# Kernel tuning notes

Measured on AMD Instinct MI355X. Metric: run time of the kernel, lower is better.

The kernel has to match this reference:

```python
import jax, jax.numpy as jnp
import numpy as np

NLAYER = 4
H = 0.1


def tv_norm(X, eps=1e-3):
    # mean-center and L2-normalize each channel over the node/edge dim
    X = X - jnp.mean(X, axis=1, keepdims=True)
    return X / jnp.sqrt(jnp.sum(X * X, axis=1, keepdims=True) + eps)


def setup_inputs() -> dict:
    key = jax.random.key(0)
    ks = jax.random.split(key, 12)
    nIn, nopenN, nopenE, nclose = 128, 128, 128, 128
    nN, nE = 50000, 500000
    xn = jax.random.normal(ks[0], (nIn, nN), dtype=jnp.float32)
    xe = jax.random.normal(ks[1], (nIn, nE), dtype=jnp.float32)
    iInd = jax.random.randint(ks[2], (nE,), 0, nN)
    jInd = jax.random.randint(ks[3], (nE,), 0, nN)
    KNopen = jax.random.uniform(ks[4], (nopenN, nIn), dtype=jnp.float32) * 0.1
    KEopen = jax.random.uniform(ks[5], (nopenE, nIn), dtype=jnp.float32) * 0.1
    KNclose = jax.random.uniform(ks[6], (nclose, nopenN), dtype=jnp.float32) * 0.1
    KEclose = jax.random.uniform(ks[7], (nclose, nopenE), dtype=jnp.float32) * 0.1
    KN = jax.random.uniform(ks[8], (NLAYER, nopenE, nopenN), dtype=jnp.float32) * 0.001
    KE = jax.random.uniform(ks[9], (NLAYER, nopenN, nopenE), dtype=jnp.float32) * 0.001
    return {"xn": xn, "xe": xe, "iInd": iInd, "jInd": jInd,
            "KNopen": KNopen, "KEopen": KEopen, "KNclose": KNclose,
            "KEclose": KEclose, "KN": KN, "KE": KE}


def reference(xn, xe, iInd, jInd, KNopen, KEopen, KNclose, KEclose, KN, KE):
    nN = xn.shape[1]

    def node_grad(x):           # [d, nN] -> [d, nE]
        return x[:, iInd] - x[:, jInd]

    def edge_div(e):            # [d, nE] -> [d, nN]
        z = jnp.zeros((e.shape[0], nN), dtype=e.dtype)
        return z.at[:, iInd].add(e).at[:, jInd].add(-e)

    xn = KNopen @ xn            # [nopenN, nN]
    xe = KEopen @ xe            # [nopenE, nE]
    for i in range(NLAYER):
        Ai = tv_norm(KN[i] @ node_grad(xn))          # [nopenE, nE]
        xe = xe + H * jax.nn.relu(Ai)
        Bi = tv_norm(jax.nn.relu(KE[i] @ edge_div(xe)))  # [nopenN, nN]
        xn = xn + H * jax.nn.relu(Bi)
    xn = KNclose @ xn
    xe = KNclose @ xe  # note: original code uses KNclose for xe as well
    return (xn, xe)
```

## Files before the change

kernel.cpp:

```cpp
#include <hip/hip_runtime.h>


#define HSTEP 0.1f
#define TVEPS 1e-3f

typedef __attribute__((ext_vector_type(8))) short short8v;
typedef __attribute__((ext_vector_type(4))) float f32x4;

__device__ inline float4 f4z() { return make_float4(0.f, 0.f, 0.f, 0.f); }

__device__ inline unsigned short f2bf(float x) {
  unsigned u = __float_as_uint(x);
  unsigned r = (u + 0x7fffu + ((u >> 16) & 1u)) >> 16;
  return (unsigned short)r;
}
__device__ inline float bf2f(unsigned short h) {
  return __uint_as_float(((unsigned)h) << 16);
}

__global__ __launch_bounds__(256) void pack6(const float* __restrict__ KNopen,
                                             const float* __restrict__ KEopen,
                                             const float* __restrict__ KN,
                                             unsigned short* __restrict__ dst) {
  const int idx = blockIdx.x * 256 + threadIdx.x;
  const int m = blockIdx.y;
  const int o = idx >> 7, k = idx & 127;
  const float* src;
  if (m == 0) src = KNopen;
  else if (m == 1) src = KEopen;
  else src = KN + (m - 2) * 16384;
  const float val = src[o * 128 + k];
  const unsigned short hi = f2bf(val);
  const unsigned short lo = f2bf(val - bf2f(hi));
  const int lane = (o & 15) + 16 * ((k >> 3) & 3);
  const int base =
      m * 32768 + (k >> 5) * 8192 + (o >> 4) * 512 + lane * 8 + (k & 7);
  dst[base] = hi;
  dst[base + 4096] = lo;
}

__global__ __launch_bounds__(256) void prep_close_w(
    const float* __restrict__ KNclose, const float* __restrict__ KEopen,
    unsigned short* __restrict__ Apack) {
  const int idx = blockIdx.x * 256 + threadIdx.x;
  const int p = idx >> 14, ok = idx & 16383;
  const int o = ok >> 7, k = ok & 127;
  float val;
  if (p == 0) {
    float s = 0.f;
    for (int m = 0; m < 128; ++m)
      s = fmaf(KNclose[o * 128 + m], KEopen[m * 128 + k], s);
    val = s;
  } else {
    val = KNclose[o * 128 + k];
  }
  const unsigned short hi = f2bf(val);
  const unsigned short lo = f2bf(val - bf2f(hi));
  const int chunk = p * 4 + (k >> 5);
  const int lane = (o & 15) + 16 * ((k >> 3) & 3);
  const int base = chunk * 8192 + (o >> 4) * 512 + lane * 8 + (k & 7);
  Apack[base] = hi;
  Apack[base + 4096] = lo;
}

__global__ __launch_bounds__(256, 2) void gemm_e_mfma(
    const float* __restrict__ X, const unsigned short* __restrict__ Wp,
    const int N, float* __restrict__ Yt) {
  __shared__ float4 Asf[1024];
  const int tid = threadIdx.x;
  const int l = tid & 63, w = tid >> 6;
  const int er = l & 15, kg = l >> 4;
  const long e0 = (long)blockIdx.x * 128;

  f32x4 acc[8][2];
#pragma unroll
  for (int of = 0; of < 8; ++of)
#pragma unroll
    for (int f = 0; f < 2; ++f) acc[of][f] = (f32x4){0.f, 0.f, 0.f, 0.f};

  long e_f[2];
  bool ev[2];
#pragma unroll
  for (int f = 0; f < 2; ++f) {
    long e = e0 + 32 * w + 16 * f + er;
    ev[f] = (e < N);
    e_f[f] = ev[f] ? e : (long)(N - 1);
  }

  const short8v* Ap = (const short8v*)Asf;

  for (int ks = 0; ks < 4; ++ks) {
    const float4* src = (const float4*)Wp + ks * 1024;
    __syncthreads();
    Asf[tid] = src[tid];
    Asf[tid + 256] = src[tid + 256];
    Asf[tid + 512] = src[tid + 512];
    Asf[tid + 768] = src[tid + 768];
    __syncthreads();

    short8v bh[2], bl[2];
#pragma unroll
    for (int f = 0; f < 2; ++f) {
      const float* col = X + e_f[f];
      const int kbase = 32 * ks + 8 * kg;
      float xv[8];
#pragma unroll
      for (int j = 0; j < 8; ++j) xv[j] = col[(long)(kbase + j) * N];
#pragma unroll
      for (int j = 0; j < 8; ++j) {
        const unsigned short h = f2bf(xv[j]);
        const unsigned short lo = f2bf(xv[j] - bf2f(h));
        bh[f][j] = (short)h;
        bl[f][j] = (short)lo;
      }
    }

#pragma unroll
    for (int of = 0; of < 8; ++of) {
      const short8v ah = Ap[of * 64 + l];
      const short8v al = Ap[512 + of * 64 + l];
#pragma unroll
      for (int f = 0; f < 2; ++f) {
        acc[of][f] =
            __builtin_amdgcn_mfma_f32_16x16x32_bf16(ah, bh[f], acc[of][f], 0, 0, 0);
        acc[of][f] =
            __builtin_amdgcn_mfma_f32_16x16x32_bf16(ah, bl[f], acc[of][f], 0, 0, 0);
        acc[of][f] =
            __builtin_amdgcn_mfma_f32_16x16x32_bf16(al, bh[f], acc[of][f], 0, 0, 0);
      }
    }
  }

#pragma unroll
  for (int of = 0; of < 8; ++of) {
#pragma unroll
    for (int f = 0; f < 2; ++f) {
      if (!ev[f]) continue;
      *(f32x4*)&Yt[e_f[f] * 128 + of * 16 + 4 * kg] = acc[of][f];
    }
  }
}

template <int MODE>
__global__ __launch_bounds__(256, 2) void gemm_n_mfma(
    const float* __restrict__ X, const unsigned short* __restrict__ Wp,
    const int N, float* __restrict__ Y) {
  __shared__ float4 Asf[1024];
  const int tid = threadIdx.x;
  const int l = tid & 63, w = tid >> 6;
  const int er = l & 15, kg = l >> 4;
  const long n0 = (long)blockIdx.x * 128;

  f32x4 acc[8][2];
#pragma unroll
  for (int of = 0; of < 8; ++of)
#pragma unroll
    for (int f = 0; f < 2; ++f) acc[of][f] = (f32x4){0.f, 0.f, 0.f, 0.f};

  long n_f[2];
  bool nv[2];
#pragma unroll
  for (int f = 0; f < 2; ++f) {
    long n = n0 + 32 * w + 16 * f + er;
    nv[f] = (n < N);
    n_f[f] = nv[f] ? n : (long)(N - 1);
  }

  const short8v* Ap = (const short8v*)Asf;

  for (int ks = 0; ks < 4; ++ks) {
    const float4* src = (const float4*)Wp + ks * 1024;
    __syncthreads();
    Asf[tid] = src[tid];
    Asf[tid + 256] = src[tid + 256];
    Asf[tid + 512] = src[tid + 512];
    Asf[tid + 768] = src[tid + 768];
    __syncthreads();

    short8v bh[2], bl[2];
#pragma unroll
    for (int f = 0; f < 2; ++f) {
      const float* row = X + n_f[f] * 128 + 32 * ks + 8 * kg;
      const float4 v0 = *(const float4*)row;
      const float4 v1 = *(const float4*)(row + 4);
      float xv[8] = {v0.x, v0.y, v0.z, v0.w, v1.x, v1.y, v1.z, v1.w};
#pragma unroll
      for (int j = 0; j < 8; ++j) {
        const unsigned short h = f2bf(xv[j]);
        const unsigned short lo = f2bf(xv[j] - bf2f(h));
        bh[f][j] = (short)h;
        bl[f][j] = (short)lo;
      }
    }

#pragma unroll
    for (int of = 0; of < 8; ++of) {
      const short8v ah = Ap[of * 64 + l];
      const short8v al = Ap[512 + of * 64 + l];
#pragma unroll
      for (int f = 0; f < 2; ++f) {
        acc[of][f] =
            __builtin_amdgcn_mfma_f32_16x16x32_bf16(ah, bh[f], acc[of][f], 0, 0, 0);
        acc[of][f] =
            __builtin_amdgcn_mfma_f32_16x16x32_bf16(ah, bl[f], acc[of][f], 0, 0, 0);
        acc[of][f] =
            __builtin_amdgcn_mfma_f32_16x16x32_bf16(al, bh[f], acc[of][f], 0, 0, 0);
      }
    }
  }

  if (MODE == 0) {
#pragma unroll
    for (int of = 0; of < 8; ++of) {
#pragma unroll
      for (int f = 0; f < 2; ++f) {
        if (!nv[f]) continue;
        *(f32x4*)&Y[n_f[f] * 128 + of * 16 + 4 * kg] = acc[of][f];
      }
    }
  } else {
#pragma unroll
    for (int of = 0; of < 8; ++of) {
#pragma unroll
      for (int f = 0; f < 2; ++f) {
        if (!nv[f]) continue;
#pragma unroll
        for (int r = 0; r < 4; ++r) {
          const long o = of * 16 + 4 * kg + r;
          Y[o * N + n_f[f]] = acc[of][f][r];
        }
      }
    }
  }
}

__global__ __launch_bounds__(256, 2) void gemm_n1(
    const float* __restrict__ X, const float* __restrict__ Kmat, const int N,
    float* __restrict__ Y, float* __restrict__ statS,
    float* __restrict__ statQ) {
  __shared__ float Xs[64 * 33];
  __shared__ float Ks[32 * 132];
  __shared__ float red[2 * 128 * 17];
  const int tid = threadIdx.x;
  const int ng = tid & 15, og = tid >> 4;
  const long n0 = (long)blockIdx.x * 64;

  float acc[4][8];
#pragma unroll
  for (int q = 0; q < 4; ++q)
#pragma unroll
    for (int j = 0; j < 8; ++j) acc[q][j] = 0.f;

  for (int kc = 0; kc < 128; kc += 32) {
#pragma unroll
    for (int i = 0; i < 2; ++i) {
      int f4i = tid + 256 * i;
      int n = f4i >> 3, c4 = (f4i & 7) << 2;
      long gn = n0 + n;
      float4 v = f4z();
      if (gn < N) v = *(const float4*)&X[gn * 128 + kc + c4];
      Xs[n * 33 + c4 + 0] = v.x;
      Xs[n * 33 + c4 + 1] = v.y;
      Xs[n * 33 + c4 + 2] = v.z;
      Xs[n * 33 + c4 + 3] = v.w;
    }
#pragma unroll
    for (int i = 0; i < 4; ++i) {
      int f4i = tid + 256 * i;
      int o = f4i >> 3, c4 = (f4i & 7) << 2;
      float4 v = *(const float4*)&Kmat[o * 128 + kc + c4];
      Ks[(c4 + 0) * 132 + o] = v.x;
      Ks[(c4 + 1) * 132 + o] = v.y;
      Ks[(c4 + 2) * 132 + o] = v.z;
      Ks[(c4 + 3) * 132 + o] = v.w;
    }
    __syncthreads();
#pragma unroll
    for (int kk = 0; kk < 32; ++kk) {
      float xv[4];
#pragma unroll
      for (int q = 0; q < 4; ++q) xv[q] = Xs[(4 * ng + q) * 33 + kk];
      const float4 k0 = *(const float4*)&Ks[kk * 132 + 8 * og];
      const float4 k1 = *(const float4*)&Ks[kk * 132 + 8 * og + 4];
      float kv[8] = {k0.x, k0.y, k0.z, k0.w, k1.x, k1.y, k1.z, k1.w};
#pragma unroll
      for (int q = 0; q < 4; ++q)
#pragma unroll
        for (int j = 0; j < 8; ++j) acc[q][j] = fmaf(xv[q], kv[j], acc[q][j]);
    }
    __syncthreads();
  }

#pragma unroll
  for (int q = 0; q < 4; ++q)
#pragma unroll
    for (int j = 0; j < 8; ++j) acc[q][j] = fmaxf(acc[q][j], 0.f);
#pragma unroll
  for (int q = 0; q < 4; ++q) {
    long n = n0 + 4 * ng + q;
    if (n < N) {
      *(float4*)&Y[n * 128 + 8 * og] =
          make_float4(acc[q][0], acc[q][1], acc[q][2], acc[q][3]);
      *(float4*)&Y[n * 128 + 8 * og + 4] =
          make_float4(acc[q][4], acc[q][5], acc[q][6], acc[q][7]);
    }
  }
  float* redS = red;
  float* redQ = red + 128 * 17;
#pragma unroll
  for (int j = 0; j < 8; ++j) {
    int o = 8 * og + j;
    float s = acc[0][j] + acc[1][j] + acc[2][j] + acc[3][j];
    float qq = acc[0][j] * acc[0][j] + acc[1][j] * acc[1][j] +
               acc[2][j] * acc[2][j] + acc[3][j] * acc[3][j];
    redS[o * 17 + ng] = s;
    redQ[o * 17 + ng] = qq;
  }
  __syncthreads();
  if (tid < 128) {
    float s = 0.f, qq = 0.f;
#pragma unroll
    for (int g = 0; g < 16; ++g) {
      s += redS[tid * 17 + g];
      qq += redQ[tid * 17 + g];
    }
    atomicAdd(&statS[tid], s);
    atomicAdd(&statQ[tid], qq);
  }
}

__global__ __launch_bounds__(256, 2) void close_edge_mfma(
    const float* __restrict__ xe, const float* __restrict__ Sacc,
    const unsigned short* __restrict__ Apack, const int nE,
    float* __restrict__ out) {
  __shared__ float4 Asf[1024];
  const int tid = threadIdx.x;
  const int l = tid & 63, w = tid >> 6;
  const int er = l & 15;
  const int kg = l >> 4;
  const long e0 = (long)blockIdx.x * 128;

  f32x4 acc[8][2];
#pragma unroll
  for (int of = 0; of < 8; ++of)
#pragma unroll
    for (int f = 0; f < 2; ++f) acc[of][f] = (f32x4){0.f, 0.f, 0.f, 0.f};

  long e_f[2];
  bool ev[2];
#pragma unroll
  for (int f = 0; f < 2; ++f) {
    long e = e0 + 32 * w + 16 * f + er;
    ev[f] = (e < nE);
    e_f[f] = ev[f] ? e : (long)(nE - 1);
  }

  const short8v* Ap = (const short8v*)Asf;

  for (int p = 0; p < 2; ++p) {
    for (int ks = 0; ks < 4; ++ks) {
      const float4* src = (const float4*)Apack + (p * 4 + ks) * 1024;
      __syncthreads();
      Asf[tid] = src[tid];
      Asf[tid + 256] = src[tid + 256];
      Asf[tid + 512] = src[tid + 512];
      Asf[tid + 768] = src[tid + 768];
      __syncthreads();

      short8v bh[2], bl[2];
#pragma unroll
      for (int f = 0; f < 2; ++f) {
        float xv[8];
        if (p == 0) {
          const float* col = xe + e_f[f];
          const int kbase = 32 * ks + 8 * kg;
#pragma unroll
          for (int j = 0; j < 8; ++j) xv[j] = col[(long)(kbase + j) * nE];
        } else {
          const float* row = Sacc + e_f[f] * 128 + 32 * ks + 8 * kg;
          const float4 v0 = *(const float4*)row;
          const float4 v1 = *(const float4*)(row + 4);
          xv[0] = v0.x; xv[1] = v0.y; xv[2] = v0.z; xv[3] = v0.w;
          xv[4] = v1.x; xv[5] = v1.y; xv[6] = v1.z; xv[7] = v1.w;
        }
#pragma unroll
        for (int j = 0; j < 8; ++j) {
          const unsigned short h = f2bf(xv[j]);
          const unsigned short lo = f2bf(xv[j] - bf2f(h));
          bh[f][j] = (short)h;
          bl[f][j] = (short)lo;
        }
      }

#pragma unroll
      for (int of = 0; of < 8; ++of) {
        const short8v ah = Ap[of * 64 + l];
        const short8v al = Ap[512 + of * 64 + l];
#pragma unroll
        for (int f = 0; f < 2; ++f) {
          acc[of][f] =
              __builtin_amdgcn_mfma_f32_16x16x32_bf16(ah, bh[f], acc[of][f], 0, 0, 0);
          acc[of][f] =
              __builtin_amdgcn_mfma_f32_16x16x32_bf16(ah, bl[f], acc[of][f], 0, 0, 0);
          acc[of][f] =
              __builtin_amdgcn_mfma_f32_16x16x32_bf16(al, bh[f], acc[of][f], 0, 0, 0);
        }
      }
    }
  }

#pragma unroll
  for (int of = 0; of < 8; ++of) {
#pragma unroll
    for (int f = 0; f < 2; ++f) {
      if (!ev[f]) continue;
      const long e = e_f[f];
#pragma unroll
      for (int r = 0; r < 4; ++r) {
        const long o = of * 16 + 4 * kg + r;
        out[o * nE + e] = acc[of][f][r];
      }
    }
  }
}

__global__ __launch_bounds__(256) void count_deg(const int* __restrict__ iInd,
                                                 const int* __restrict__ jInd,
                                                 const int nE,
                                                 int* __restrict__ cnt) {
  const int e = blockIdx.x * 256 + threadIdx.x;
  if (e >= nE) return;
  atomicAdd(&cnt[iInd[e]], 1);
  atomicAdd(&cnt[jInd[e]], 1);
}

__global__ __launch_bounds__(1024) void scan_rowptr(const int* __restrict__ cnt,
                                                    int* __restrict__ rp,
                                                    const int nN) {
  __shared__ int buf[1024];
  __shared__ int carry;
  const int tid = threadIdx.x;
  if (tid == 0) {
    carry = 0;
    rp[0] = 0;
  }
  __syncthreads();
  for (int base = 0; base < nN; base += 1024) {
    int idx = base + tid;
    int v = (idx < nN) ? cnt[idx] : 0;
    buf[tid] = v;
    __syncthreads();
    for (int off = 1; off < 1024; off <<= 1) {
      int t = (tid >= off) ? buf[tid - off] : 0;
      __syncthreads();
      buf[tid] += t;
      __syncthreads();
    }
    if (idx < nN) rp[idx + 1] = buf[tid] + carry;
    __syncthreads();
    if (tid == 0) carry += buf[1023];
    __syncthreads();
  }
}

__global__ __launch_bounds__(256) void fill_adj(const int* __restrict__ iInd,
                                                const int* __restrict__ jInd,
                                                const int nE,
                                                const int* __restrict__ rp,
                                                int* __restrict__ cur,
                                                int* __restrict__ adj) {
  const int e = blockIdx.x * 256 + threadIdx.x;
  if (e >= nE) return;
  const int ii = iInd[e], jj = jInd[e];
  int s1 = atomicAdd(&cur[ii], 1);
  adj[rp[ii] + s1] = (e << 1);
  int s2 = atomicAdd(&cur[jj], 1);
  adj[rp[jj] + s2] = (e << 1) | 1;
}

template <bool OPEN>
__global__ __launch_bounds__(256) void div_gather(
    const float* __restrict__ E, const int* __restrict__ rp,
    const int* __restrict__ adj, const float* __restrict__ D0,
    float* __restrict__ D, const int nN) {
  const int cg = threadIdx.x & 31, slot = threadIdx.x >> 5;
  const long n = (long)blockIdx.x * 8 + slot;
  if (n >= nN) return;
  const float4* E4 = (const float4*)E;
  float4 acc;
  if (OPEN) {
    acc = f4z();
  } else {
    acc = ((const float4*)D0)[n * 32 + cg];
  }
  const int b = rp[n], en = rp[n + 1];
  for (int k = b; k < en; ++k) {
    const int ent = adj[k];
    const long e = ent >> 1;
    const float4 v = E4[e * 32 + cg];
    if (ent & 1) {
      acc.x -= v.x; acc.y -= v.y; acc.z -= v.z; acc.w -= v.w;
    } else {
      acc.x += v.x; acc.y += v.y; acc.z += v.z; acc.w += v.w;
    }
  }
  ((float4*)D)[n * 32 + cg] = acc;
}

__global__ __launch_bounds__(256) void edge_pass1(
    const float* __restrict__ W, const int* __restrict__ iInd,
    const int* __restrict__ jInd, const int nE, float* __restrict__ statS,
    float* __restrict__ statQ) {
  __shared__ float4 rs[256];
  __shared__ float4 rq[256];
  const int tid = threadIdx.x;
  const int cg = tid & 31, slot = tid >> 5;
  const float4* W4 = (const float4*)W;
  float4 s = f4z(), q = f4z();
  long start = (long)blockIdx.x * 512;
  long end = start + 512;
  if (end > nE) end = nE;
  for (long e = start + slot; e < end; e += 8) {
    const int ii = iInd[e], jj = jInd[e];
    const float4 wi = W4[(long)ii * 32 + cg];
    const float4 wj = W4[(long)jj * 32 + cg];
    const float y0 = wi.x - wj.x, y1 = wi.y - wj.y;
    const float y2 = wi.z - wj.z, y3 = wi.w - wj.w;
    s.x += y0; s.y += y1; s.z += y2; s.w += y3;
    q.x = fmaf(y0, y0, q.x); q.y = fmaf(y1, y1, q.y);
    q.z = fmaf(y2, y2, q.z); q.w = fmaf(y3, y3, q.w);
  }
  rs[tid] = s;
  rq[tid] = q;
  __syncthreads();
  if (tid < 32) {
    float4 S = rs[tid], Q = rq[tid];
#pragma unroll
    for (int g = 1; g < 8; ++g) {
      float4 a = rs[tid + 32 * g], b = rq[tid + 32 * g];
      S.x += a.x; S.y += a.y; S.z += a.z; S.w += a.w;
      Q.x += b.x; Q.y += b.y; Q.z += b.z; Q.w += b.w;
    }
    atomicAdd(&statS[tid * 4 + 0], S.x);
    atomicAdd(&statS[tid * 4 + 1], S.y);
    atomicAdd(&statS[tid * 4 + 2], S.z);
    atomicAdd(&statS[tid * 4 + 3], S.w);
    atomicAdd(&statQ[tid * 4 + 0], Q.x);
    atomicAdd(&statQ[tid * 4 + 1], Q.y);
    atomicAdd(&statQ[tid * 4 + 2], Q.z);
    atomicAdd(&statQ[tid * 4 + 3], Q.w);
  }
}

template <bool FIRST>
__global__ __launch_bounds__(256) void edge_pass2(
    const float* __restrict__ W, const int* __restrict__ iInd,
    const int* __restrict__ jInd, const int nE, const float* __restrict__ mean,
    const float* __restrict__ rsig, float* __restrict__ Sacc) {
  const int tid = threadIdx.x;
  const int cg = tid & 31, slot = tid >> 5;
  const float4 mu = *(const float4*)&mean[cg * 4];
  const float4 sg = *(const float4*)&rsig[cg * 4];
  const float4* W4 = (const float4*)W;
  float4* S4 = (float4*)Sacc;
  long start = (long)blockIdx.x * 512;
  long end = start + 512;
  if (end > nE) end = nE;
  for (long e = start + slot; e < end; e += 8) {
    const int ii = iInd[e], jj = jInd[e];
    const float4 wi = W4[(long)ii * 32 + cg];
    const float4 wj = W4[(long)jj * 32 + cg];
    const float r0 = fmaxf(((wi.x - wj.x) - mu.x) * sg.x, 0.f) * HSTEP;
    const float r1 = fmaxf(((wi.y - wj.y) - mu.y) * sg.y, 0.f) * HSTEP;
    const float r2 = fmaxf(((wi.z - wj.z) - mu.z) * sg.z, 0.f) * HSTEP;
    const float r3 = fmaxf(((wi.w - wj.w) - mu.w) * sg.w, 0.f) * HSTEP;
    float4 sv;
    if (FIRST) {
      sv = make_float4(r0, r1, r2, r3);
    } else {
      sv = S4[e * 32 + cg];
      sv.x += r0; sv.y += r1; sv.z += r2; sv.w += r3;
    }
    S4[e * 32 + cg] = sv;
  }
}

__global__ void fin_stats(const float* __restrict__ S,
                          const float* __restrict__ Q, const float cnt,
                          float* __restrict__ mean, float* __restrict__ rsig) {
  const int c = threadIdx.x;
  const float mu = S[c] / cnt;
  const float var = Q[c] - cnt * mu * mu;
  mean[c] = mu;
  rsig[c] = rsqrtf(var + TVEPS);
}

__global__ __launch_bounds__(256) void apply_node(
    const float* __restrict__ R, const float* __restrict__ mean,
    const float* __restrict__ rsig, float* __restrict__ xnt,
    const long total4) {
  const long idx = (long)blockIdx.x * 256 + threadIdx.x;
  if (idx >= total4) return;
  const int o4 = (int)(idx & 31) * 4;
  const float4 m = *(const float4*)&mean[o4];
  const float4 s = *(const float4*)&rsig[o4];
  const float4 r = ((const float4*)R)[idx];
  float4 x = ((float4*)xnt)[idx];
  x.x += HSTEP * fmaxf((r.x - m.x) * s.x, 0.f);
  x.y += HSTEP * fmaxf((r.y - m.y) * s.y, 0.f);
  x.z += HSTEP * fmaxf((r.z - m.z) * s.z, 0.f);
  x.w += HSTEP * fmaxf((r.w - m.w) * s.w, 0.f);
  ((float4*)xnt)[idx] = x;
}

extern "C" void kernel_launch(void* const* d_in, const int* in_sizes, int n_in,
                              void* d_out, int out_size, void* d_ws,
                              size_t ws_size, hipStream_t stream) {
  const float* xn = (const float*)d_in[0];
  const float* xe = (const float*)d_in[1];
  const int* iInd = (const int*)d_in[2];
  const int* jInd = (const int*)d_in[3];
  const float* KNopen = (const float*)d_in[4];
  const float* KEopen = (const float*)d_in[5];
  const float* KNclose = (const float*)d_in[6];
  const float* KN = (const float*)d_in[8];
  const float* KE = (const float*)d_in[9];

  const int nN = in_sizes[0] / 128;
  const int nE = in_sizes[2];

  float* out_xn = (float*)d_out;
  float* out_xe = (float*)d_out + (size_t)128 * nN;

  float* ws = (float*)d_ws;
  size_t off = 0;
  float* Sacc = ws + off; off += (size_t)nE * 128;
  float* W    = ws + off; off += (size_t)nN * 128;
  float* Dacc = ws + off; off += (size_t)nN * 128;
  float* D0   = ws + off; off += (size_t)nN * 128;
  float* xnt  = ws + off; off += (size_t)nN * 128;
  unsigned short* Apack = (unsigned short*)(ws + off); off += 32768;
  unsigned short* Wpack = (unsigned short*)(ws + off); off += 98304;
  float* stats = ws + off; off += 1024;
  float* statS = stats;        float* statQ = stats + 128;
  float* meanE = stats + 256;  float* rsigE = stats + 384;
  float* statS2 = stats + 512; float* statQ2 = stats + 640;
  float* meanN = stats + 768;  float* rsigN = stats + 896;
  int* rp  = (int*)(ws + off); off += (size_t)nN + 1 + 63;
  int* cnt = (int*)(ws + off); off += nN;
  int* cur = (int*)(ws + off); off += nN;
  int* adj = (int*)(ws + off); off += (size_t)2 * nE;
  float* Eopen = Sacc;
  float* R = W;

  const int gN = (nN + 63) / 64;
  const int gNm = (nN + 127) / 128;
  const int gEm = (nE + 127) / 128;
  const int gP = (nE + 511) / 512;
  const int gEdge = (nE + 255) / 256;
  const int gGath = (nN + 7) / 8;
  const int gA = (int)(((long)nN * 32 + 255) / 256);

  hipMemsetAsync(cnt, 0, (size_t)nN * sizeof(int), stream);
  hipMemsetAsync(cur, 0, (size_t)nN * sizeof(int), stream);
  count_deg<<<gEdge, 256, 0, stream>>>(iInd, jInd, nE, cnt);
  scan_rowptr<<<1, 1024, 0, stream>>>(cnt, rp, nN);
  fill_adj<<<gEdge, 256, 0, stream>>>(iInd, jInd, nE, rp, cur, adj);

  pack6<<<dim3(64, 6), 256, 0, stream>>>(KNopen, KEopen, KN, Wpack);
  prep_close_w<<<128, 256, 0, stream>>>(KNclose, KEopen, Apack);

  gemm_e_mfma<<<gNm, 256, 0, stream>>>(xn, Wpack, nN, xnt);
  gemm_e_mfma<<<gEm, 256, 0, stream>>>(xe, Wpack + 32768, nE, Eopen);
  div_gather<true><<<gGath, 256, 0, stream>>>(Eopen, rp, adj, nullptr, D0, nN);

  for (int layer = 0; layer < 4; ++layer) {
    hipMemsetAsync(stats, 0, 1024 * sizeof(float), stream);
    gemm_n_mfma<0><<<gNm, 256, 0, stream>>>(
        xnt, Wpack + (size_t)(2 + layer) * 32768, nN, W);
    edge_pass1<<<gP, 256, 0, stream>>>(W, iInd, jInd, nE, statS, statQ);
    fin_stats<<<1, 128, 0, stream>>>(statS, statQ, (float)nE, meanE, rsigE);
    if (layer == 0)
      edge_pass2<true><<<gP, 256, 0, stream>>>(W, iInd, jInd, nE, meanE, rsigE,
                                               Sacc);
    else
      edge_pass2<false><<<gP, 256, 0, stream>>>(W, iInd, jInd, nE, meanE,
                                                rsigE, Sacc);
    div_gather<false><<<gGath, 256, 0, stream>>>(Sacc, rp, adj, D0, Dacc, nN);
    gemm_n1<<<gN, 256, 0, stream>>>(Dacc, KE + layer * 16384, nN, R, statS2,
                                    statQ2);
    fin_stats<<<1, 128, 0, stream>>>(statS2, statQ2, (float)nN, meanN, rsigN);
    apply_node<<<gA, 256, 0, stream>>>(R, meanN, rsigN, xnt, (long)nN * 32);
  }

  gemm_n_mfma<2><<<gNm, 256, 0, stream>>>(xnt, Apack + 32768, nN, out_xn);
  close_edge_mfma<<<gEm, 256, 0, stream>>>(xe, Sacc, Apack, nE, out_xe);
}
```

Before: 2.979 ms.

## Fuse edge activation into node divergence gather and defer edge accumulation

Drops the per-layer edge_pass2 write of the 500k x 128 edge accumulator. The divergence is now accumulated directly into Dacc by recomputing each incident edge's normalized ReLU from the node features W, using a new neighbor-index array built in fill_adj. The per-layer W matrices and stats are kept, stored in the output buffer as scratch, and a single compute_sacc kernel builds the final edge accumulator before the close GEMM. This trades several full edge-sized read/write passes per layer for redundant per-edge recomputation (each edge is evaluated twice in the gather) and a larger adjacency array.

```diff
diff --git a/kernel.cpp b/kernel.cpp
--- a/kernel.cpp
+++ b/kernel.cpp
@@ -468,31 +468,27 @@
                                                 const int nE,
                                                 const int* __restrict__ rp,
                                                 int* __restrict__ cur,
-                                                int* __restrict__ adj) {
+                                                int* __restrict__ adj,
+                                                int* __restrict__ adjO) {
   const int e = blockIdx.x * 256 + threadIdx.x;
   if (e >= nE) return;
   const int ii = iInd[e], jj = jInd[e];
   int s1 = atomicAdd(&cur[ii], 1);
   adj[rp[ii] + s1] = (e << 1);
+  adjO[rp[ii] + s1] = jj;
   int s2 = atomicAdd(&cur[jj], 1);
   adj[rp[jj] + s2] = (e << 1) | 1;
-}
-
-template <bool OPEN>
-__global__ __launch_bounds__(256) void div_gather(
+  adjO[rp[jj] + s2] = ii;
+}
+
+__global__ __launch_bounds__(256) void div_open(
     const float* __restrict__ E, const int* __restrict__ rp,
-    const int* __restrict__ adj, const float* __restrict__ D0,
-    float* __restrict__ D, const int nN) {
+    const int* __restrict__ adj, float* __restrict__ Dacc, const int nN) {
   const int cg = threadIdx.x & 31, slot = threadIdx.x >> 5;
   const long n = (long)blockIdx.x * 8 + slot;
   if (n >= nN) return;
   const float4* E4 = (const float4*)E;
-  float4 acc;
-  if (OPEN) {
-    acc = f4z();
-  } else {
-    acc = ((const float4*)D0)[n * 32 + cg];
-  }
+  float4 acc = f4z();
   const int b = rp[n], en = rp[n + 1];
   for (int k = b; k < en; ++k) {
     const int ent = adj[k];
@@ -504,7 +500,72 @@
       acc.x += v.x; acc.y += v.y; acc.z += v.z; acc.w += v.w;
     }
   }
-  ((float4*)D)[n * 32 + cg] = acc;
+  ((float4*)Dacc)[n * 32 + cg] = acc;
+}
+
+__global__ __launch_bounds__(256) void div_fused(
+    const float* __restrict__ W, const int* __restrict__ rp,
+    const int* __restrict__ adj, const int* __restrict__ adjO,
+    const float* __restrict__ mean, const float* __restrict__ rsig,
+    float* __restrict__ Dacc, const int nN) {
+  const int cg = threadIdx.x & 31, slot = threadIdx.x >> 5;
+  const long n = (long)blockIdx.x * 8 + slot;
+  if (n >= nN) return;
+  const float4* W4 = (const float4*)W;
+  const float4 mu = *(const float4*)&mean[cg * 4];
+  const float4 sg = *(const float4*)&rsig[cg * 4];
+  const float4 wn = W4[n * 32 + cg];
+  float4 acc = ((const float4*)Dacc)[n * 32 + cg];
+  const int b = rp[n], en = rp[n + 1];
+  for (int k = b; k < en; ++k) {
+    const float s = (adj[k] & 1) ? -1.f : 1.f;
+    const long o = adjO[k];
+    const float4 wo = W4[o * 32 + cg];
+    const float t0 = fmaxf((s * (wn.x - wo.x) - mu.x) * sg.x, 0.f);
+    const float t1 = fmaxf((s * (wn.y - wo.y) - mu.y) * sg.y, 0.f);
+    const float t2 = fmaxf((s * (wn.z - wo.z) - mu.z) * sg.z, 0.f);
+    const float t3 = fmaxf((s * (wn.w - wo.w) - mu.w) * sg.w, 0.f);
+    const float sh = s * HSTEP;
+    acc.x = fmaf(sh, t0, acc.x);
+    acc.y = fmaf(sh, t1, acc.y);
+    acc.z = fmaf(sh, t2, acc.z);
+    acc.w = fmaf(sh, t3, acc.w);
+  }
+  ((float4*)Dacc)[n * 32 + cg] = acc;
+}
+
+__global__ __launch_bounds__(256) void compute_sacc(
+    const float* __restrict__ Wb, const long lstr4,
+    const int* __restrict__ iInd, const int* __restrict__ jInd, const int nE,
+    const float* __restrict__ meanAll, const float* __restrict__ rsigAll,
+    float* __restrict__ Sacc) {
+  const int tid = threadIdx.x;
+  const int cg = tid & 31, slot = tid >> 5;
+  float4 mu[4], sg[4];
+#pragma unroll
+  for (int l = 0; l < 4; ++l) {
+    mu[l] = *(const float4*)&meanAll[l * 128 + cg * 4];
+    sg[l] = *(const float4*)&rsigAll[l * 128 + cg * 4];
+  }
+  const float4* W4 = (const float4*)Wb;
+  float4* S4 = (float4*)Sacc;
+  long start = (long)blockIdx.x * 512;
+  long end = start + 512;
+  if (end > nE) end = nE;
+  for (long e = start + slot; e < end; e += 8) {
+    const long ii = iInd[e], jj = jInd[e];
+    float4 acc = f4z();
+#pragma unroll
+    for (int l = 0; l < 4; ++l) {
+      const float4 wi = W4[l * lstr4 + ii * 32 + cg];
+      const float4 wj = W4[l * lstr4 + jj * 32 + cg];
+      acc.x += HSTEP * fmaxf(((wi.x - wj.x) - mu[l].x) * sg[l].x, 0.f);
+      acc.y += HSTEP * fmaxf(((wi.y - wj.y) - mu[l].y) * sg[l].y, 0.f);
+      acc.z += HSTEP * fmaxf(((wi.z - wj.z) - mu[l].z) * sg[l].z, 0.f);
+      acc.w += HSTEP * fmaxf(((wi.w - wj.w) - mu[l].w) * sg[l].w, 0.f);
+    }
+    S4[e * 32 + cg] = acc;
+  }
 }
 
 __global__ __launch_bounds__(256) void edge_pass1(
@@ -552,39 +613,6 @@
   }
 }
 
-template <bool FIRST>
-__global__ __launch_bounds__(256) void edge_pass2(
-    const float* __restrict__ W, const int* __restrict__ iInd,
-    const int* __restrict__ jInd, const int nE, const float* __restrict__ mean,
-    const float* __restrict__ rsig, float* __restrict__ Sacc) {
-  const int tid = threadIdx.x;
-  const int cg = tid & 31, slot = tid >> 5;
-  const float4 mu = *(const float4*)&mean[cg * 4];
-  const float4 sg = *(const float4*)&rsig[cg * 4];
-  const float4* W4 = (const float4*)W;
-  float4* S4 = (float4*)Sacc;
-  long start = (long)blockIdx.x * 512;
-  long end = start + 512;
-  if (end > nE) end = nE;
-  for (long e = start + slot; e < end; e += 8) {
-    const int ii = iInd[e], jj = jInd[e];
-    const float4 wi = W4[(long)ii * 32 + cg];
-    const float4 wj = W4[(long)jj * 32 + cg];
-    const float r0 = fmaxf(((wi.x - wj.x) - mu.x) * sg.x, 0.f) * HSTEP;
-    const float r1 = fmaxf(((wi.y - wj.y) - mu.y) * sg.y, 0.f) * HSTEP;
-    const float r2 = fmaxf(((wi.z - wj.z) - mu.z) * sg.z, 0.f) * HSTEP;
-    const float r3 = fmaxf(((wi.w - wj.w) - mu.w) * sg.w, 0.f) * HSTEP;
-    float4 sv;
-    if (FIRST) {
-      sv = make_float4(r0, r1, r2, r3);
-    } else {
-      sv = S4[e * 32 + cg];
-      sv.x += r0; sv.y += r1; sv.z += r2; sv.w += r3;
-    }
-    S4[e * 32 + cg] = sv;
-  }
-}
-
 __global__ void fin_stats(const float* __restrict__ S,
                           const float* __restrict__ Q, const float cnt,
                           float* __restrict__ mean, float* __restrict__ rsig) {
@@ -635,23 +663,25 @@
   float* ws = (float*)d_ws;
   size_t off = 0;
   float* Sacc = ws + off; off += (size_t)nE * 128;
-  float* W    = ws + off; off += (size_t)nN * 128;
   float* Dacc = ws + off; off += (size_t)nN * 128;
-  float* D0   = ws + off; off += (size_t)nN * 128;
   float* xnt  = ws + off; off += (size_t)nN * 128;
   unsigned short* Apack = (unsigned short*)(ws + off); off += 32768;
   unsigned short* Wpack = (unsigned short*)(ws + off); off += 98304;
-  float* stats = ws + off; off += 1024;
+  float* stats = ws + off; off += 2048;
   float* statS = stats;        float* statQ = stats + 128;
-  float* meanE = stats + 256;  float* rsigE = stats + 384;
-  float* statS2 = stats + 512; float* statQ2 = stats + 640;
-  float* meanN = stats + 768;  float* rsigN = stats + 896;
-  int* rp  = (int*)(ws + off); off += (size_t)nN + 1 + 63;
-  int* cnt = (int*)(ws + off); off += nN;
-  int* cur = (int*)(ws + off); off += nN;
-  int* adj = (int*)(ws + off); off += (size_t)2 * nE;
+  float* statS2 = stats + 256; float* statQ2 = stats + 384;
+  float* meanN = stats + 512;  float* rsigN = stats + 640;
+  float* meanEall = stats + 768;
+  float* rsigEall = stats + 1280;
+  int* rp   = (int*)(ws + off); off += (size_t)nN + 1 + 63;
+  int* cnt  = (int*)(ws + off); off += nN;
+  int* cur  = (int*)(ws + off); off += nN;
+  int* adj  = (int*)(ws + off); off += (size_t)2 * nE;
+  int* adjO = (int*)(ws + off); off += (size_t)2 * nE;
   float* Eopen = Sacc;
-  float* R = W;
+
+  float* Wb = out_xe;
+  float* R  = out_xe + (size_t)4 * nN * 128;
 
   const int gN = (nN + 63) / 64;
   const int gNm = (nN + 127) / 128;
@@ -660,39 +690,40 @@
   const int gEdge = (nE + 255) / 256;
   const int gGath = (nN + 7) / 8;
   const int gA = (int)(((long)nN * 32 + 255) / 256);
+  const long lstr4 = (long)nN * 32;
 
   hipMemsetAsync(cnt, 0, (size_t)nN * sizeof(int), stream);
   hipMemsetAsync(cur, 0, (size_t)nN * sizeof(int), stream);
   count_deg<<<gEdge, 256, 0, stream>>>(iInd, jInd, nE, cnt);
   scan_rowptr<<<1, 1024, 0, stream>>>(cnt, rp, nN);
-  fill_adj<<<gEdge, 256, 0, stream>>>(iInd, jInd, nE, rp, cur, adj);
+  fill_adj<<<gEdge, 256, 0, stream>>>(iInd, jInd, nE, rp, cur, adj, adjO);
 
   pack6<<<dim3(64, 6), 256, 0, stream>>>(KNopen, KEopen, KN, Wpack);
   prep_close_w<<<128, 256, 0, stream>>>(KNclose, KEopen, Apack);
 
   gemm_e_mfma<<<gNm, 256, 0, stream>>>(xn, Wpack, nN, xnt);
   gemm_e_mfma<<<gEm, 256, 0, stream>>>(xe, Wpack + 32768, nE, Eopen);
-  div_gather<true><<<gGath, 256, 0, stream>>>(Eopen, rp, adj, nullptr, D0, nN);
+  div_open<<<gGath, 256, 0, stream>>>(Eopen, rp, adj, Dacc, nN);
 
   for (int layer = 0; layer < 4; ++layer) {
-    hipMemsetAsync(stats, 0, 1024 * sizeof(float), stream);
+    float* Wl = Wb + (size_t)layer * nN * 128;
+    float* meanE = meanEall + 128 * layer;
+    float* rsigE = rsigEall + 128 * layer;
+    hipMemsetAsync(stats, 0, 512 * sizeof(float), stream);
     gemm_n_mfma<0><<<gNm, 256, 0, stream>>>(
-        xnt, Wpack + (size_t)(2 + layer) * 32768, nN, W);
-    edge_pass1<<<gP, 256, 0, stream>>>(W, iInd, jInd, nE, statS, statQ);
+        xnt, Wpack + (size_t)(2 + layer) * 32768, nN, Wl);
+    edge_pass1<<<gP, 256, 0, stream>>>(Wl, iInd, jInd, nE, statS, statQ);
     fin_stats<<<1, 128, 0, stream>>>(statS, statQ, (float)nE, meanE, rsigE);
-    if (layer == 0)
-      edge_pass2<true><<<gP, 256, 0, stream>>>(W, iInd, jInd, nE, meanE, rsigE,
-                                               Sacc);
-    else
-      edge_pass2<false><<<gP, 256, 0, stream>>>(W, iInd, jInd, nE, meanE,
-                                                rsigE, Sacc);
-    div_gather<false><<<gGath, 256, 0, stream>>>(Sacc, rp, adj, D0, Dacc, nN);
+    div_fused<<<gGath, 256, 0, stream>>>(Wl, rp, adj, adjO, meanE, rsigE,
+                                         Dacc, nN);
     gemm_n1<<<gN, 256, 0, stream>>>(Dacc, KE + layer * 16384, nN, R, statS2,
                                     statQ2);
     fin_stats<<<1, 128, 0, stream>>>(statS2, statQ2, (float)nN, meanN, rsigN);
     apply_node<<<gA, 256, 0, stream>>>(R, meanN, rsigN, xnt, (long)nN * 32);
   }
 
+  compute_sacc<<<gP, 256, 0, stream>>>(Wb, lstr4, iInd, jInd, nE, meanEall,
+                                       rsigEall, Sacc);
   gemm_n_mfma<2><<<gNm, 256, 0, stream>>>(xnt, Apack + 32768, nN, out_xn);
   close_edge_mfma<<<gEm, 256, 0, stream>>>(xe, Sacc, Apack, nE, out_xe);
 }
```

Measured after the change: 2.596 ms. -12.9%, faster.
